# Optimization experiments

Measured on AMD Instinct MI355X. Metric: run time of the kernel, lower is better.

Reference implementation:

```python
import jax, jax.numpy as jnp
import numpy as np

N = 50000       # nodes
E = 800000      # edges (before self-loops)
F_IN = 128      # in_channels
HID = 32        # hidden_channels per head
HEADS = 4
OUT = 16        # out_channels
NEG_SLOPE = 0.2 # PyG GATConv leaky_relu slope
EPS = 1e-16     # PyG softmax denominator eps
BN_EPS = 1e-5


def setup_inputs() -> dict:
    key = jax.random.key(0)
    ks = jax.random.split(key, 20)
    rn = lambda k, shp, s=0.1: (jax.random.normal(k, shp, jnp.float32) * s)
    x = jax.random.normal(ks[0], (N, F_IN), jnp.float32)
    edge_index = jax.random.randint(ks[1], (2, E), 0, N, dtype=jnp.int32)
    D0 = HEADS * HID  # 128
    return {
        "x": x, "edge_index": edge_index,
        # layer 0: GATConv(F_IN -> HID, heads=HEADS, concat=True)
        "W0": rn(ks[2], (F_IN, HEADS * HID)), "as0": rn(ks[3], (HEADS, HID)),
        "ad0": rn(ks[4], (HEADS, HID)), "b0": jnp.zeros((D0,), jnp.float32),
        "g0": jnp.ones((D0,), jnp.float32) + rn(ks[5], (D0,), 0.05),
        "be0": rn(ks[6], (D0,), 0.05),
        # layer 1: GATConv(D0 -> HID, heads=HEADS, concat=True)
        "W1": rn(ks[7], (D0, HEADS * HID)), "as1": rn(ks[8], (HEADS, HID)),
        "ad1": rn(ks[9], (HEADS, HID)), "b1": jnp.zeros((D0,), jnp.float32),
        "g1": jnp.ones((D0,), jnp.float32) + rn(ks[10], (D0,), 0.05),
        "be1": rn(ks[11], (D0,), 0.05),
        # layer 2: GATConv(D0 -> OUT, heads=1, concat=False)
        "W2": rn(ks[12], (D0, OUT)), "as2": rn(ks[13], (1, OUT)),
        "ad2": rn(ks[14], (1, OUT)), "b2": jnp.zeros((OUT,), jnp.float32),
    }


def _gat(x, src, dst, W, a_s, a_d, b, heads, ch, concat):
    n = x.shape[0]
    h = (x @ W).reshape(n, heads, ch)                       # [N,H,C]
    score_s = (h * a_s).sum(-1)                             # [N,H]
    score_d = (h * a_d).sum(-1)                             # [N,H]
    e = jax.nn.leaky_relu(score_s[src] + score_d[dst], NEG_SLOPE)  # [E,H]
    emax = jax.ops.segment_max(e, dst, num_segments=n)
    emax = jnp.where(jnp.isfinite(emax), emax, 0.0)
    p = jnp.exp(e - emax[dst])
    denom = jax.ops.segment_sum(p, dst, num_segments=n)
    alpha = p / (denom[dst] + EPS)                          # segment softmax over dst
    out = jax.ops.segment_sum(h[src] * alpha[:, :, None], dst, num_segments=n)
    out = out.reshape(n, heads * ch) if concat else out.mean(axis=1)
    return out + b


def _bn(x, g, be):
    m = x.mean(0)
    v = x.var(0)
    return (x - m) * jax.lax.rsqrt(v + BN_EPS) * g + be


def reference(x, edge_index, W0, as0, ad0, b0, g0, be0,
              W1, as1, ad1, b1, g1, be1, W2, as2, ad2, b2):
    n = x.shape[0]
    loop = jnp.arange(n, dtype=edge_index.dtype)
    src = jnp.concatenate([edge_index[0], loop])  # PyG add_self_loops
    dst = jnp.concatenate([edge_index[1], loop])
    h = _gat(x, src, dst, W0, as0, ad0, b0, HEADS, HID, True)
    h = jax.nn.elu(_bn(h, g0, be0))                 # dropout disabled (eval)
    h = _gat(h, src, dst, W1, as1, ad1, b1, HEADS, HID, True)
    h = jax.nn.elu(_bn(h, g1, be1))
    return _gat(h, src, dst, W2, as2, ad2, b2, 1, OUT, False)
```

## Files before the change

kernel.cpp:

```cpp
#include <hip/hip_runtime.h>
#include <hip/hip_bf16.h>
#include <math.h>

#define NEG_SLOPE 0.2f
#define EPS_SM 1e-16f
#define BN_EPS 1e-5f
#define CHUNKS 256

typedef __attribute__((ext_vector_type(8))) short bf16x8;
typedef __attribute__((ext_vector_type(4))) float f32x4;

__device__ __forceinline__ float lrelu(float x) { return x > 0.f ? x : NEG_SLOPE * x; }
__device__ __forceinline__ ushort f2bf(float f) {
    uint u = __float_as_uint(f);
    return (ushort)((u + 0x7FFFu + ((u >> 16) & 1u)) >> 16);
}
__device__ __forceinline__ float bfl(uint u) { return __uint_as_float(u << 16); }
__device__ __forceinline__ float bfh(uint u) { return __uint_as_float(u & 0xFFFF0000u); }

__global__ void pack_w(const float* __restrict__ W0, const float* __restrict__ W1,
                       const float* __restrict__ W2, ushort* __restrict__ P0,
                       ushort* __restrict__ P1, ushort* __restrict__ P2,
                       float* __restrict__ sums) {
    int i = blockIdx.x * blockDim.x + threadIdx.x;
    if (i < 8192) sums[i] = 0.f;
    const float* W;
    ushort* P;
    int NC, s;
    if (i < 16384) { W = W0; P = P0; NC = 128; s = i; }
    else if (i < 32768) { W = W1; P = P1; NC = 128; s = i - 16384; }
    else if (i < 34816) { W = W2; P = P2; NC = 16; s = i - 32768; }
    else return;
    int k = s / NC, col = s % NC;
    int CT = NC >> 4;
    int dst = (((k >> 5) * CT + (col >> 4)) << 9) +
              (((col & 15) | (((k >> 3) & 3) << 4)) << 3) + (k & 7);
    P[dst] = f2bf(W[s]);
}

__global__ __launch_bounds__(256) void bucket_scatter(const int* __restrict__ src,
                                                      const int* __restrict__ dst, int E,
                                                      const int* __restrict__ base,
                                                      uint* __restrict__ bpack, int nbuck) {
    __shared__ int cur[256];
    int blk = blockIdx.x, tid = threadIdx.x;
    if (tid < nbuck) cur[tid] = base[tid * CHUNKS + blk];
    __syncthreads();
    int e0 = (int)(((long)E * blk) >> 8);
    int e1 = (int)(((long)E * (blk + 1)) >> 8);
    for (int i = e0 + tid; i < e1; i += 256) {
        int d = dst[i];
        int p = atomicAdd(&cur[d >> 8], 1);
        bpack[p] = ((uint)src[i] << 8) | (uint)(d & 255);
    }
}

__global__ __launch_bounds__(256) void fine_csr(const uint* __restrict__ bpack,
                                                const int* __restrict__ base, int E, int n,
                                                int* __restrict__ offs, int* __restrict__ srcs,
                                                int nbuck) {
    __shared__ int cnt[256];
    __shared__ int wsum[4];
    int bk = blockIdx.x, tid = threadIdx.x;
    int ebase = base[bk * CHUNKS];
    int eend = base[(bk + 1) * CHUNKS];
    cnt[tid] = 0;
    __syncthreads();
    for (int i = ebase + tid; i < eend; i += 256) atomicAdd(&cnt[bpack[i] & 255], 1);
    __syncthreads();
    int lane = tid & 63, w = tid >> 6;
    int v = cnt[tid];
    int incl = v;
#pragma unroll
    for (int d = 1; d < 64; d <<= 1) {
        int t = __shfl_up(incl, d, 64);
        if (lane >= d) incl += t;
    }
    if (lane == 63) wsum[w] = incl;
    __syncthreads();
    int wbase = 0;
    for (int j = 0; j < w; ++j) wbase += wsum[j];
    int excl = wbase + incl - v;
    int node = bk * 256 + tid;
    if (node < n) offs[node] = ebase + excl;
    cnt[tid] = ebase + excl;
    __syncthreads();
    for (int i = ebase + tid; i < eend; i += 256) {
        uint pk = bpack[i];
        int p = atomicAdd(&cnt[pk & 255], 1);
        srcs[p] = (int)(pk >> 8);
    }
    if (bk == nbuck - 1 && tid == 0) offs[n] = E;
}

template <int NC, int HEADS, bool XBN, bool BCFUSE>
__global__ __launch_bounds__(64) void gemm_mfma(
    const void* __restrict__ Xv, const ushort* __restrict__ Wp, ushort* __restrict__ Hb,
    int n, const float* __restrict__ sumsP, const float* __restrict__ g,
    const float* __restrict__ be, const float* __restrict__ as_, const float* __restrict__ ad_,
    float* __restrict__ ss, float* __restrict__ sd,
    const int* __restrict__ dstE, int E, int* __restrict__ hist, int nbuck) {
    int tid = threadIdx.x;
    constexpr int CT = NC / 16;
    constexpr int FPH = NC / HEADS / 16;
    __shared__ __align__(16) ushort Xb[16 * 128];
    __shared__ float ssl[16 * HEADS], sdl[16 * HEADS];
    if constexpr (BCFUSE) {
        if ((int)blockIdx.x < CHUNKS) {
            int* h = (int*)Xb;
            for (int j = tid; j < 256; j += 64) h[j] = 0;
            __syncthreads();
            int blk = blockIdx.x;
            int e0 = (int)(((long)E * blk) >> 8);
            int e1 = (int)(((long)E * (blk + 1)) >> 8);
            for (int i = e0 + tid; i < e1; i += 64) atomicAdd(&h[dstE[i] >> 8], 1);
            __syncthreads();
            for (int j = tid; j < nbuck; j += 64) hist[j * CHUNKS + blk] = h[j];
            return;
        }
    }
    int bid = BCFUSE ? ((int)blockIdx.x - CHUNKS) : (int)blockIdx.x;
    int row0 = bid * 16;
    if constexpr (!XBN) {
        const float* X = (const float*)Xv;
#pragma unroll
        for (int i = 0; i < 8; ++i) {
            int idx = tid + i * 64;
            int row = idx >> 5, q = idx & 31;
            int gr = row0 + row;
            float4 v = make_float4(0.f, 0.f, 0.f, 0.f);
            if (gr < n) v = ((const float4*)(X + (long)gr * 128))[q];
            ushort4 p = make_ushort4(f2bf(v.x), f2bf(v.y), f2bf(v.z), f2bf(v.w));
            int s = (q >> 1) ^ (row & 15);
            *(ushort4*)&Xb[row * 128 + s * 8 + (q & 1) * 4] = p;
        }
    } else {
        const ushort* X = (const ushort*)Xv;
        int c8 = (tid & 15) * 8;
        float inv_n = 1.f / (float)n;
        float bm[8], bs[8], bb[8];
#pragma unroll
        for (int j = 0; j < 8; ++j) {
            int ch = c8 + j;
            float m = sumsP[ch * 16] * inv_n;
            float vv = fmaxf(sumsP[(128 + ch) * 16] * inv_n - m * m, 0.f);
            bm[j] = m;
            bs[j] = rsqrtf(vv + BN_EPS) * g[ch];
            bb[j] = be[ch];
        }
#pragma unroll
        for (int i = 0; i < 4; ++i) {
            int idx = tid + i * 64;
            int row = idx >> 4, g8 = idx & 15;
            int gr = row0 + row;
            uint4 v = make_uint4(0, 0, 0, 0);
            if (gr < n) v = ((const uint4*)(X + (long)gr * 128))[g8];
            float a, b;
#define BNE(comp, j0)                                                  \
    a = bfl(comp); b = bfh(comp);                                      \
    a = (a - bm[j0]) * bs[j0] + bb[j0]; a = a > 0.f ? a : expm1f(a);   \
    b = (b - bm[j0 + 1]) * bs[j0 + 1] + bb[j0 + 1];                    \
    b = b > 0.f ? b : expm1f(b);                                       \
    comp = (uint)f2bf(a) | ((uint)f2bf(b) << 16);
            BNE(v.x, 0) BNE(v.y, 2) BNE(v.z, 4) BNE(v.w, 6)
#undef BNE
            int s = g8 ^ (row & 15);
            *(uint4*)&Xb[row * 128 + s * 8] = v;
        }
    }
    __syncthreads();
    int lane = tid;
    int lrow = lane & 15, lhi = lane >> 4;
    f32x4 zero = {0.f, 0.f, 0.f, 0.f};
    f32x4 acc[CT];
#pragma unroll
    for (int f = 0; f < CT; ++f) acc[f] = zero;
    const ushort* xr = &Xb[lrow * 128];
#pragma unroll
    for (int ks = 0; ks < 4; ++ks) {
        int kg = ks * 4 + lhi;
        bf16x8 a = *(const bf16x8*)&xr[(kg ^ lrow) << 3];
#pragma unroll
        for (int f = 0; f < CT; ++f) {
            bf16x8 b = *(const bf16x8*)&Wp[((ks * CT + f) * 64 + lane) * 8];
            acc[f] = __builtin_amdgcn_mfma_f32_16x16x32_bf16(a, b, acc[f], 0, 0, 0);
        }
    }
    __syncthreads();
#pragma unroll
    for (int f = 0; f < CT; ++f)
#pragma unroll
        for (int j = 0; j < 4; ++j)
            Xb[(lhi * 4 + j) * NC + f * 16 + lrow] = f2bf(acc[f][j]);
    float asv[CT], adv[CT];
#pragma unroll
    for (int f = 0; f < CT; ++f) {
        asv[f] = as_[f * 16 + lrow];
        adv[f] = ad_[f * 16 + lrow];
    }
#pragma unroll
    for (int h = 0; h < HEADS; ++h) {
        float ps[4] = {}, pd[4] = {};
#pragma unroll
        for (int fi = 0; fi < FPH; ++fi) {
            int f = h * FPH + fi;
#pragma unroll
            for (int j = 0; j < 4; ++j) {
                ps[j] = fmaf(acc[f][j], asv[f], ps[j]);
                pd[j] = fmaf(acc[f][j], adv[f], pd[j]);
            }
        }
#pragma unroll
        for (int j = 0; j < 4; ++j) {
#pragma unroll
            for (int d = 1; d < 16; d <<= 1) {
                ps[j] += __shfl_xor(ps[j], d, 64);
                pd[j] += __shfl_xor(pd[j], d, 64);
            }
            if (lrow == 0) {
                ssl[(lhi * 4 + j) * HEADS + h] = ps[j];
                sdl[(lhi * 4 + j) * HEADS + h] = pd[j];
            }
        }
    }
    __syncthreads();
    constexpr int NU = 16 * NC / 8;
#pragma unroll
    for (int i = 0; i < (NU + 63) / 64; ++i) {
        int idx = tid + i * 64;
        if (idx < NU) {
            int row = idx / (NC / 8), c8i = idx % (NC / 8);
            int gr = row0 + row;
            if (gr < n) ((uint4*)&Hb[(long)gr * NC])[c8i] = ((const uint4*)Xb)[idx];
        }
    }
    if (tid < 16 * HEADS) {
        int row = tid / HEADS, hh = tid % HEADS;
        int gr = row0 + row;
        if (gr < n) {
            ss[(long)gr * HEADS + hh] = ssl[tid];
            sd[(long)gr * HEADS + hh] = sdl[tid];
        }
    }
}

__global__ __launch_bounds__(1024) void scan_kernel(const int* __restrict__ deg,
                                                    int* __restrict__ offs, int n) {
    __shared__ int wsum[16];
    __shared__ int wpre[16];
    __shared__ int carry_s;
    int tid = threadIdx.x;
    int lane = tid & 63;
    int w = tid >> 6;
    if (tid == 0) carry_s = 0;
    __syncthreads();
    int nv = (n + 3) >> 2;
    for (int base = 0; base < nv; base += 1024) {
        int carry = carry_s;
        int gi = base + tid;
        int e0 = gi * 4;
        int4 v = make_int4(0, 0, 0, 0);
        if (e0 + 3 < n) {
            v = ((const int4*)deg)[gi];
        } else if (e0 < n) {
            v.x = deg[e0];
            if (e0 + 1 < n) v.y = deg[e0 + 1];
            if (e0 + 2 < n) v.z = deg[e0 + 2];
        }
        int tsum = v.x + v.y + v.z + v.w;
        int incl = tsum;
#pragma unroll
        for (int d = 1; d < 64; d <<= 1) {
            int t = __shfl_up(incl, d, 64);
            if (lane >= d) incl += t;
        }
        if (lane == 63) wsum[w] = incl;
        __syncthreads();
        if (w == 0 && lane < 16) {
            int s = wsum[lane];
#pragma unroll
            for (int d = 1; d < 16; d <<= 1) {
                int t = __shfl_up(s, d, 64);
                if (lane >= d) s += t;
            }
            wpre[lane] = s;
        }
        __syncthreads();
        int wbase = (w == 0) ? 0 : wpre[w - 1];
        int ex = carry + wbase + incl - tsum;
        if (e0 < n) {
            int4 o;
            o.x = ex;
            o.y = ex + v.x;
            o.z = o.y + v.y;
            o.w = o.z + v.z;
            if (e0 + 3 < n) {
                ((int4*)offs)[gi] = o;
            } else {
                offs[e0] = o.x;
                if (e0 + 1 < n) offs[e0 + 1] = o.y;
                if (e0 + 2 < n) offs[e0 + 2] = o.z;
            }
        }
        __syncthreads();
        if (tid == 1023) carry_s = carry + wpre[15];
        __syncthreads();
    }
    if (tid == 0) offs[n] = carry_s;
}

__global__ __launch_bounds__(256) void gat_gather4(
    const uint* __restrict__ hb, const float* __restrict__ ss, const float* __restrict__ sd,
    const int* __restrict__ offs, const int* __restrict__ srcs,
    const float* __restrict__ bias, ushort* __restrict__ outb, int n) {
    int wid = threadIdx.x >> 6;
    int lane = threadIdx.x & 63;
    int node = blockIdx.x * 4 + wid;
    if (node >= n) return;
    int off = offs[node];
    int dg = offs[node + 1] - off;
    int grp = lane >> 4;
    int ll = lane & 15;
    int hd = ll >> 2;
    float sdn = sd[node * 4 + hd];
    float es = lrelu(ss[node * 4 + hd] + sdn);
    const uint* hrow = hb + ll * 4;
    float acc[8] = {};
    float sm = 0.f;
    int i = grp;
    for (; i + 4 < dg; i += 8) {
        int s0 = srcs[off + i];
        int s1 = srcs[off + i + 4];
        float w0 = __expf(lrelu(ss[s0 * 4 + hd] + sdn));
        float w1 = __expf(lrelu(ss[s1 * 4 + hd] + sdn));
        uint4 h0 = *(const uint4*)(hrow + (long)s0 * 64);
        uint4 h1 = *(const uint4*)(hrow + (long)s1 * 64);
        sm += w0 + w1;
        acc[0] = fmaf(w0, bfl(h0.x), acc[0]); acc[0] = fmaf(w1, bfl(h1.x), acc[0]);
        acc[1] = fmaf(w0, bfh(h0.x), acc[1]); acc[1] = fmaf(w1, bfh(h1.x), acc[1]);
        acc[2] = fmaf(w0, bfl(h0.y), acc[2]); acc[2] = fmaf(w1, bfl(h1.y), acc[2]);
        acc[3] = fmaf(w0, bfh(h0.y), acc[3]); acc[3] = fmaf(w1, bfh(h1.y), acc[3]);
        acc[4] = fmaf(w0, bfl(h0.z), acc[4]); acc[4] = fmaf(w1, bfl(h1.z), acc[4]);
        acc[5] = fmaf(w0, bfh(h0.z), acc[5]); acc[5] = fmaf(w1, bfh(h1.z), acc[5]);
        acc[6] = fmaf(w0, bfl(h0.w), acc[6]); acc[6] = fmaf(w1, bfl(h1.w), acc[6]);
        acc[7] = fmaf(w0, bfh(h0.w), acc[7]); acc[7] = fmaf(w1, bfh(h1.w), acc[7]);
    }
    for (; i < dg; i += 4) {
        int s = srcs[off + i];
        float w = __expf(lrelu(ss[s * 4 + hd] + sdn));
        sm += w;
        uint4 hv = *(const uint4*)(hrow + (long)s * 64);
        acc[0] = fmaf(w, bfl(hv.x), acc[0]);
        acc[1] = fmaf(w, bfh(hv.x), acc[1]);
        acc[2] = fmaf(w, bfl(hv.y), acc[2]);
        acc[3] = fmaf(w, bfh(hv.y), acc[3]);
        acc[4] = fmaf(w, bfl(hv.z), acc[4]);
        acc[5] = fmaf(w, bfh(hv.z), acc[5]);
        acc[6] = fmaf(w, bfl(hv.w), acc[6]);
        acc[7] = fmaf(w, bfh(hv.w), acc[7]);
    }
#pragma unroll
    for (int j = 0; j < 8; ++j) {
        acc[j] += __shfl_xor(acc[j], 16, 64);
        acc[j] += __shfl_xor(acc[j], 32, 64);
    }
    sm += __shfl_xor(sm, 16, 64);
    sm += __shfl_xor(sm, 32, 64);
    float wS = __expf(es);
    sm += wS;
    uint4 hvS = *(const uint4*)(hrow + (long)node * 64);
    acc[0] = fmaf(wS, bfl(hvS.x), acc[0]);
    acc[1] = fmaf(wS, bfh(hvS.x), acc[1]);
    acc[2] = fmaf(wS, bfl(hvS.y), acc[2]);
    acc[3] = fmaf(wS, bfh(hvS.y), acc[3]);
    acc[4] = fmaf(wS, bfl(hvS.z), acc[4]);
    acc[5] = fmaf(wS, bfh(hvS.z), acc[5]);
    acc[6] = fmaf(wS, bfl(hvS.w), acc[6]);
    acc[7] = fmaf(wS, bfh(hvS.w), acc[7]);
    float inv = 1.f / (sm + EPS_SM);
    if (grp == 0) {
        float4 bA = *(const float4*)&bias[ll * 8];
        float4 bB = *(const float4*)&bias[ll * 8 + 4];
        uint4 p;
        p.x = (uint)f2bf(acc[0] * inv + bA.x) | ((uint)f2bf(acc[1] * inv + bA.y) << 16);
        p.y = (uint)f2bf(acc[2] * inv + bA.z) | ((uint)f2bf(acc[3] * inv + bA.w) << 16);
        p.z = (uint)f2bf(acc[4] * inv + bB.x) | ((uint)f2bf(acc[5] * inv + bB.y) << 16);
        p.w = (uint)f2bf(acc[6] * inv + bB.z) | ((uint)f2bf(acc[7] * inv + bB.w) << 16);
        *(uint4*)&outb[(long)node * 128 + ll * 8] = p;
    }
}

__global__ __launch_bounds__(256) void gat_gather1(
    const uint* __restrict__ hb2, const float* __restrict__ ss, const float* __restrict__ sd,
    const int* __restrict__ offs, const int* __restrict__ srcs,
    const float* __restrict__ bias, float* __restrict__ out, int n) {
    int wid = threadIdx.x >> 6;
    int lane = threadIdx.x & 63;
    int node = blockIdx.x * 4 + wid;
    if (node >= n) return;
    int off = offs[node];
    int dg = offs[node + 1] - off;
    int grp = lane >> 3;
    int ll = lane & 7;
    float sdn = sd[node];
    float es = lrelu(ss[node] + sdn);
    float a0 = 0.f, a1 = 0.f, sm = 0.f;
    int i = grp;
    for (; i + 8 < dg; i += 16) {
        int s0 = srcs[off + i];
        int s1 = srcs[off + i + 8];
        float w0 = __expf(lrelu(ss[s0] + sdn));
        float w1 = __expf(lrelu(ss[s1] + sdn));
        uint h0 = hb2[s0 * 8 + ll];
        uint h1 = hb2[s1 * 8 + ll];
        sm += w0 + w1;
        a0 = fmaf(w0, bfl(h0), a0); a0 = fmaf(w1, bfl(h1), a0);
        a1 = fmaf(w0, bfh(h0), a1); a1 = fmaf(w1, bfh(h1), a1);
    }
    for (; i < dg; i += 8) {
        int s = srcs[off + i];
        float w = __expf(lrelu(ss[s] + sdn));
        sm += w;
        uint hv = hb2[s * 8 + ll];
        a0 = fmaf(w, bfl(hv), a0);
        a1 = fmaf(w, bfh(hv), a1);
    }
#pragma unroll
    for (int d = 8; d <= 32; d <<= 1) {
        a0 += __shfl_xor(a0, d, 64);
        a1 += __shfl_xor(a1, d, 64);
        sm += __shfl_xor(sm, d, 64);
    }
    float wS = __expf(es);
    sm += wS;
    uint hvS = hb2[node * 8 + ll];
    a0 = fmaf(wS, bfl(hvS), a0);
    a1 = fmaf(wS, bfh(hvS), a1);
    float inv = 1.f / (sm + EPS_SM);
    if (grp == 0) {
        float2 o = make_float2(a0 * inv + bias[ll * 2], a1 * inv + bias[ll * 2 + 1]);
        *(float2*)&out[(long)node * 16 + ll * 2] = o;
    }
}

__global__ __launch_bounds__(256) void bn_stats_bf16(const uint4* __restrict__ X4,
                                                     float* __restrict__ sumsP, int n) {
    __shared__ float red[4096];
    int tid = threadIdx.x;
    float s[8] = {}, s2[8] = {};
    long tot = (long)n * 16;
    long T = (long)gridDim.x * 256;
    for (long i = (long)blockIdx.x * 256 + tid; i < tot; i += T) {
        uint4 v = X4[i];
        float f;
        f = bfl(v.x); s[0] += f; s2[0] = fmaf(f, f, s2[0]);
        f = bfh(v.x); s[1] += f; s2[1] = fmaf(f, f, s2[1]);
        f = bfl(v.y); s[2] += f; s2[2] = fmaf(f, f, s2[2]);
        f = bfh(v.y); s[3] += f; s2[3] = fmaf(f, f, s2[3]);
        f = bfl(v.z); s[4] += f; s2[4] = fmaf(f, f, s2[4]);
        f = bfh(v.z); s[5] += f; s2[5] = fmaf(f, f, s2[5]);
        f = bfl(v.w); s[6] += f; s2[6] = fmaf(f, f, s2[6]);
        f = bfh(v.w); s[7] += f; s2[7] = fmaf(f, f, s2[7]);
    }
#pragma unroll
    for (int j = 0; j < 8; ++j) {
        red[j * 256 + tid] = s[j];
        red[(8 + j) * 256 + tid] = s2[j];
    }
    __syncthreads();
    int ch = tid & 127, st = tid >> 7;
    int base = (st * 8 + (ch & 7)) * 256 + (ch >> 3);
    float a = 0.f;
#pragma unroll
    for (int rep = 0; rep < 16; ++rep) a += red[base + rep * 16];
    atomicAdd(&sumsP[tid * 16], a);
}

extern "C" void kernel_launch(void* const* d_in, const int* in_sizes, int n_in,
                              void* d_out, int out_size, void* d_ws, size_t ws_size,
                              hipStream_t stream) {
    const float* x = (const float*)d_in[0];
    const int* ei = (const int*)d_in[1];
    const float* W0 = (const float*)d_in[2];
    const float* as0 = (const float*)d_in[3];
    const float* ad0 = (const float*)d_in[4];
    const float* b0 = (const float*)d_in[5];
    const float* g0 = (const float*)d_in[6];
    const float* be0 = (const float*)d_in[7];
    const float* W1 = (const float*)d_in[8];
    const float* as1 = (const float*)d_in[9];
    const float* ad1 = (const float*)d_in[10];
    const float* b1 = (const float*)d_in[11];
    const float* g1 = (const float*)d_in[12];
    const float* be1 = (const float*)d_in[13];
    const float* W2 = (const float*)d_in[14];
    const float* as2 = (const float*)d_in[15];
    const float* ad2 = (const float*)d_in[16];
    const float* b2 = (const float*)d_in[17];

    int n = in_sizes[0] / 128;
    int E = in_sizes[1] / 2;
    const int* srcA = ei;
    const int* dstA = ei + E;
    int nbuck = (n + 255) >> 8;

    char* base = (char*)d_ws;
    auto alloc = [&](size_t bytes) {
        char* p = base;
        base += (bytes + 255) & ~(size_t)255;
        return p;
    };
    ushort* hb = (ushort*)alloc((size_t)n * 128 * 2);
    ushort* actb = (ushort*)alloc((size_t)n * 128 * 2);
    ushort* h2b = (ushort*)alloc((size_t)n * 16 * 2);
    float* ssb = (float*)alloc((size_t)n * 4 * 4);
    float* sdb = (float*)alloc((size_t)n * 4 * 4);
    float* sumsP0 = (float*)alloc(4096 * 4);
    float* sumsP1 = (float*)alloc(4096 * 4);
    int* hist = (int*)alloc(((size_t)nbuck * CHUNKS + 1) * 4);
    int* bbase = (int*)alloc(((size_t)nbuck * CHUNKS + 1) * 4);
    uint* bpack = (uint*)alloc((size_t)E * 4);
    int* offs = (int*)alloc(((size_t)n + 1) * 4);
    int* srcs = (int*)alloc((size_t)E * 4);
    ushort* Wp0 = (ushort*)alloc(16384 * 2);
    ushort* Wp1 = (ushort*)alloc(16384 * 2);
    ushort* Wp2 = (ushort*)alloc(2048 * 2);

    float* out = (float*)d_out;

    pack_w<<<136, 256, 0, stream>>>(W0, W1, W2, Wp0, Wp1, Wp2, sumsP0);

    int gGemm = (n + 15) / 16;
    int gWave = (n + 3) / 4;

    gemm_mfma<128, 4, false, true><<<CHUNKS + gGemm, 64, 0, stream>>>(
        x, Wp0, hb, n, nullptr, g0, be0, as0, ad0, ssb, sdb, dstA, E, hist, nbuck);
    scan_kernel<<<1, 1024, 0, stream>>>(hist, bbase, nbuck * CHUNKS);
    bucket_scatter<<<CHUNKS, 256, 0, stream>>>(srcA, dstA, E, bbase, bpack, nbuck);
    fine_csr<<<nbuck, 256, 0, stream>>>(bpack, bbase, E, n, offs, srcs, nbuck);

    gat_gather4<<<gWave, 256, 0, stream>>>((const uint*)hb, ssb, sdb, offs, srcs, b0, actb, n);
    bn_stats_bf16<<<256, 256, 0, stream>>>((const uint4*)actb, sumsP0, n);

    gemm_mfma<128, 4, true, false><<<gGemm, 64, 0, stream>>>(
        actb, Wp1, hb, n, sumsP0, g0, be0, as1, ad1, ssb, sdb, nullptr, 0, nullptr, 0);
    gat_gather4<<<gWave, 256, 0, stream>>>((const uint*)hb, ssb, sdb, offs, srcs, b1, actb, n);
    bn_stats_bf16<<<256, 256, 0, stream>>>((const uint4*)actb, sumsP1, n);

    gemm_mfma<16, 1, true, false><<<gGemm, 64, 0, stream>>>(
        actb, Wp2, h2b, n, sumsP1, g1, be1, as2, ad2, ssb, sdb, nullptr, 0, nullptr, 0);
    gat_gather1<<<gWave, 256, 0, stream>>>((const uint*)h2b, ssb, sdb, offs, srcs, b2, out, n);
}
```

Baseline: 215.7 us.

## Fold single-block histogram scan into bucket scatter and fine CSR kernels

After: 210.9 us. 2.3% less time.

```diff
diff --git a/kernel.cpp b/kernel.cpp
--- a/kernel.cpp
+++ b/kernel.cpp
@@ -38,13 +38,39 @@
     P[dst] = f2bf(W[s]);
 }
 
+
 __global__ __launch_bounds__(256) void bucket_scatter(const int* __restrict__ src,
                                                       const int* __restrict__ dst, int E,
-                                                      const int* __restrict__ base,
+                                                      const int* __restrict__ hist,
                                                       uint* __restrict__ bpack, int nbuck) {
     __shared__ int cur[256];
+    __shared__ int wsum[4];
     int blk = blockIdx.x, tid = threadIdx.x;
-    if (tid < nbuck) cur[tid] = base[tid * CHUNKS + blk];
+    int lane = tid & 63, w = tid >> 6;
+    int total = 0, partial = 0;
+    if (tid < nbuck) {
+        const int4* hp = (const int4*)(hist + tid * CHUNKS);
+        int nblk4 = blk >> 2;
+#pragma unroll 8
+        for (int c = 0; c < CHUNKS / 4; ++c) {
+            int4 vv = hp[c];
+            int s4 = vv.x + vv.y + vv.z + vv.w;
+            total += s4;
+            partial += (c < nblk4) ? s4 : 0;
+        }
+        for (int c = nblk4 * 4; c < blk; ++c) partial += hist[tid * CHUNKS + c];
+    }
+    int incl = total;
+#pragma unroll
+    for (int d = 1; d < 64; d <<= 1) {
+        int t = __shfl_up(incl, d, 64);
+        if (lane >= d) incl += t;
+    }
+    if (lane == 63) wsum[w] = incl;
+    __syncthreads();
+    int wbase = 0;
+    for (int j = 0; j < w; ++j) wbase += wsum[j];
+    if (tid < nbuck) cur[tid] = wbase + incl - total + partial;
     __syncthreads();
     int e0 = (int)(((long)E * blk) >> 8);
     int e1 = (int)(((long)E * (blk + 1)) >> 8);
@@ -56,19 +82,40 @@
 }
 
 __global__ __launch_bounds__(256) void fine_csr(const uint* __restrict__ bpack,
-                                                const int* __restrict__ base, int E, int n,
+                                                const int* __restrict__ hist, int E, int n,
                                                 int* __restrict__ offs, int* __restrict__ srcs,
                                                 int nbuck) {
     __shared__ int cnt[256];
     __shared__ int wsum[4];
+    __shared__ int sh_base, sh_tot;
     int bk = blockIdx.x, tid = threadIdx.x;
-    int ebase = base[bk * CHUNKS];
-    int eend = base[(bk + 1) * CHUNKS];
+    int lane = tid & 63, w = tid >> 6;
+    int acc = 0;
+    const int4* h4 = (const int4*)hist;
+    int n4 = bk * (CHUNKS / 4);
+    for (int i = tid; i < n4; i += 256) {
+        int4 vv = h4[i];
+        acc += vv.x + vv.y + vv.z + vv.w;
+    }
+#pragma unroll
+    for (int d = 32; d >= 1; d >>= 1) acc += __shfl_xor(acc, d, 64);
+    if (lane == 0) wsum[w] = acc;
+    __syncthreads();
+    if (tid == 0) sh_base = wsum[0] + wsum[1] + wsum[2] + wsum[3];
+    __syncthreads();
+    int btr = hist[bk * CHUNKS + tid];
+#pragma unroll
+    for (int d = 32; d >= 1; d >>= 1) btr += __shfl_xor(btr, d, 64);
+    if (lane == 0) wsum[w] = btr;
+    __syncthreads();
+    if (tid == 0) sh_tot = wsum[0] + wsum[1] + wsum[2] + wsum[3];
+    __syncthreads();
+    int ebase = sh_base;
+    int eend = ebase + sh_tot;
     cnt[tid] = 0;
     __syncthreads();
     for (int i = ebase + tid; i < eend; i += 256) atomicAdd(&cnt[bpack[i] & 255], 1);
     __syncthreads();
-    int lane = tid & 63, w = tid >> 6;
     int v = cnt[tid];
     int incl = v;
 #pragma unroll
@@ -242,71 +289,6 @@
             sd[(long)gr * HEADS + hh] = sdl[tid];
         }
     }
-}
-
-__global__ __launch_bounds__(1024) void scan_kernel(const int* __restrict__ deg,
-                                                    int* __restrict__ offs, int n) {
-    __shared__ int wsum[16];
-    __shared__ int wpre[16];
-    __shared__ int carry_s;
-    int tid = threadIdx.x;
-    int lane = tid & 63;
-    int w = tid >> 6;
-    if (tid == 0) carry_s = 0;
-    __syncthreads();
-    int nv = (n + 3) >> 2;
-    for (int base = 0; base < nv; base += 1024) {
-        int carry = carry_s;
-        int gi = base + tid;
-        int e0 = gi * 4;
-        int4 v = make_int4(0, 0, 0, 0);
-        if (e0 + 3 < n) {
-            v = ((const int4*)deg)[gi];
-        } else if (e0 < n) {
-            v.x = deg[e0];
-            if (e0 + 1 < n) v.y = deg[e0 + 1];
-            if (e0 + 2 < n) v.z = deg[e0 + 2];
-        }
-        int tsum = v.x + v.y + v.z + v.w;
-        int incl = tsum;
-#pragma unroll
-        for (int d = 1; d < 64; d <<= 1) {
-            int t = __shfl_up(incl, d, 64);
-            if (lane >= d) incl += t;
-        }
-        if (lane == 63) wsum[w] = incl;
-        __syncthreads();
-        if (w == 0 && lane < 16) {
-            int s = wsum[lane];
-#pragma unroll
-            for (int d = 1; d < 16; d <<= 1) {
-                int t = __shfl_up(s, d, 64);
-                if (lane >= d) s += t;
-            }
-            wpre[lane] = s;
-        }
-        __syncthreads();
-        int wbase = (w == 0) ? 0 : wpre[w - 1];
-        int ex = carry + wbase + incl - tsum;
-        if (e0 < n) {
-            int4 o;
-            o.x = ex;
-            o.y = ex + v.x;
-            o.z = o.y + v.y;
-            o.w = o.z + v.z;
-            if (e0 + 3 < n) {
-                ((int4*)offs)[gi] = o;
-            } else {
-                offs[e0] = o.x;
-                if (e0 + 1 < n) offs[e0 + 1] = o.y;
-                if (e0 + 2 < n) offs[e0 + 2] = o.z;
-            }
-        }
-        __syncthreads();
-        if (tid == 1023) carry_s = carry + wpre[15];
-        __syncthreads();
-    }
-    if (tid == 0) offs[n] = carry_s;
 }
 
 __global__ __launch_bounds__(256) void gat_gather4(
@@ -517,8 +499,7 @@
     float* sdb = (float*)alloc((size_t)n * 4 * 4);
     float* sumsP0 = (float*)alloc(4096 * 4);
     float* sumsP1 = (float*)alloc(4096 * 4);
-    int* hist = (int*)alloc(((size_t)nbuck * CHUNKS + 1) * 4);
-    int* bbase = (int*)alloc(((size_t)nbuck * CHUNKS + 1) * 4);
+    int* hist = (int*)alloc((size_t)nbuck * CHUNKS * 4);
     uint* bpack = (uint*)alloc((size_t)E * 4);
     int* offs = (int*)alloc(((size_t)n + 1) * 4);
     int* srcs = (int*)alloc((size_t)E * 4);
@@ -535,9 +516,8 @@
 
     gemm_mfma<128, 4, false, true><<<CHUNKS + gGemm, 64, 0, stream>>>(
         x, Wp0, hb, n, nullptr, g0, be0, as0, ad0, ssb, sdb, dstA, E, hist, nbuck);
-    scan_kernel<<<1, 1024, 0, stream>>>(hist, bbase, nbuck * CHUNKS);
-    bucket_scatter<<<CHUNKS, 256, 0, stream>>>(srcA, dstA, E, bbase, bpack, nbuck);
-    fine_csr<<<nbuck, 256, 0, stream>>>(bpack, bbase, E, n, offs, srcs, nbuck);
+    bucket_scatter<<<CHUNKS, 256, 0, stream>>>(srcA, dstA, E, hist, bpack, nbuck);
+    fine_csr<<<nbuck, 256, 0, stream>>>(bpack, hist, E, n, offs, srcs, nbuck);
 
     gat_gather4<<<gWave, 256, 0, stream>>>((const uint*)hb, ssb, sdb, offs, srcs, b0, actb, n);
     bn_stats_bf16<<<256, 256, 0, stream>>>((const uint4*)actb, sumsP0, n);
```
